# Kernel tuning notes

Measured on AMD Instinct MI355X. Metric: run time of the kernel, lower is better.

## Reference

```python
import jax, jax.numpy as jnp
import numpy as np

B = 1024          # sub (= obj) batch size
NUME = 20000      # num entities
NUMR = 8          # num relations
NET = 2 * NUMR + 1  # hetero edge types: r, -r, self
DIMT = 28         # time encoding dim
DIME = 100        # entity embedding dim
DIM = 200         # emb module output dim
H = 4             # history length
HEADS = 4         # GAT heads
OH = DIM // HEADS # GAT per-head out dim
N0 = 160000       # layer-0 src nodes
N1 = 40000        # layer-0 dst / layer-1 src nodes
R = 2 * B * H     # unique roots = layer-1 dst nodes
E0 = 60000        # edges per etype, layer 0
E1 = 16000        # edges per etype, layer 1
K = 500000        # copy mask entries
DIMR = 100        # relation embedding dim
HATT = 4          # self-attention heads
OA = DIM // HATT  # per-head q/k/v dim (Attention out_dim//h)
DIN0 = DIME + DIMT
DIN1 = DIM + DIMT


def setup_inputs() -> dict:
    key = jax.random.key(0)
    ks = jax.random.split(key, 48)
    ri = jax.random.randint
    nrm = lambda i, shp, s=0.05: jax.random.normal(ks[i], shp, jnp.float32) * s
    d = {}
    d['sub'] = ri(ks[0], (B,), 0, NUME)
    d['obj'] = ri(ks[1], (B,), 0, NUME)
    d['rel'] = ri(ks[2], (B,), 0, NUMR)
    d['ts'] = 1000
    d['nid0'] = ri(ks[3], (N0,), 0, NUME * 1000)
    d['root_idx'] = ri(ks[4], (2 * B * H,), 0, R)
    d['src0'] = ri(ks[5], (NET, E0), 0, N0)
    d['dst0'] = ri(ks[6], (NET, E0), 0, N1)
    d['src1'] = ri(ks[7], (NET, E1), 0, N1)
    d['dst1'] = ri(ks[8], (NET, E1), 0, R)
    d['copy_rows'] = ri(ks[9], (K,), 0, 2 * B)
    d['copy_cols'] = ri(ks[10], (K,), 0, NUME)
    # parameters
    d['emb_table'] = nrm(11, (NUME, DIME))
    d['time_freq'] = jnp.asarray(1.0 / 10 ** np.linspace(0, 9, DIMT), jnp.float32)
    d['time_phase'] = jnp.zeros((DIMT,), jnp.float32)
    d['Wg0'] = nrm(12, (NET, DIN0, HEADS, OH))
    d['al0'] = nrm(13, (NET, HEADS, OH))
    d['ar0'] = nrm(14, (NET, HEADS, OH))
    d['bg0'] = jnp.zeros((NET, DIM), jnp.float32)
    d['Wg1'] = nrm(15, (NET, DIN1, HEADS, OH))
    d['al1'] = nrm(16, (NET, HEADS, OH))
    d['ar1'] = nrm(17, (NET, HEADS, OH))
    d['bg1'] = jnp.zeros((NET, DIM), jnp.float32)
    d['ln0_w'] = jnp.ones((H * DIM,), jnp.float32)
    d['ln0_b'] = jnp.zeros((H * DIM,), jnp.float32)
    d['Wq'] = nrm(18, (HATT, DIM, OA))
    d['bq'] = jnp.zeros((HATT, OA), jnp.float32)
    d['Wv'] = nrm(19, (HATT, DIM, OA))
    d['bv'] = jnp.zeros((HATT, OA), jnp.float32)
    d['ln1_w'] = jnp.ones((H * DIM,), jnp.float32)
    d['ln1_b'] = jnp.zeros((H * DIM,), jnp.float32)
    d['Wd1'] = nrm(20, (H * DIM, DIM))
    d['bd1'] = jnp.zeros((DIM,), jnp.float32)
    d['srel_emb'] = nrm(21, (NUMR, DIMR))
    d['orel_emb'] = nrm(22, (NUMR, DIMR))
    d['Wsub'] = nrm(23, (DIM + DIMR, NUME))
    d['bsub'] = jnp.zeros((NUME,), jnp.float32)
    d['Wobj'] = nrm(24, (DIM + DIMR, NUME))
    d['bobj'] = jnp.zeros((NUME,), jnp.float32)
    d['csrel_emb'] = nrm(25, (NUMR, DIMR))
    d['corel_emb'] = nrm(26, (NUMR, DIMR))
    d['cWsub'] = nrm(27, (DIM + DIMR, NUME))
    d['cbsub'] = jnp.zeros((NUME,), jnp.float32)
    d['cWobj'] = nrm(28, (DIM + DIMR, NUME))
    d['cbobj'] = jnp.zeros((NUME,), jnp.float32)
    return d


def _temb(nid, ts, tf, tp):
    t = (ts - nid // NUME).astype(jnp.float32)
    return jnp.cos(t[:, None] * tf + tp)


def _gat(x, Wg, al, ar, bg, src, dst, nd):
    # heterogeneous GATConv over NET relation types, mean-aggregated (DGL HeteroGraphConv)
    msg = jnp.zeros((nd, HEADS, OH), x.dtype)
    for r in range(NET):
        s, d = src[r], dst[r]
        fs = jnp.einsum('ei,iho->eho', x[s], Wg[r])                     # [E,h,o] src feats per edge
        er_n = (jnp.einsum('ni,iho->nho', x[:nd], Wg[r]) * ar[r]).sum(-1)  # [nd,h]
        el = (fs * al[r]).sum(-1)                                       # [E,h]
        e = jax.nn.leaky_relu(el + er_n[d], 0.2)
        m = jax.ops.segment_max(e, d, num_segments=nd)
        a = jnp.exp(e - m[d])
        z = jax.ops.segment_sum(a, d, num_segments=nd)
        alpha = a / z[d]
        msg = msg + jax.ops.segment_sum(alpha[:, :, None] * fs, d, num_segments=nd)
    return jax.nn.relu((msg.reshape(nd, HEADS * OH) + bg.sum(0)) / NET)


def _ln(x, w, b):
    mu = x.mean(-1, keepdims=True)
    v = ((x - mu) ** 2).mean(-1, keepdims=True)
    return (x - mu) / jnp.sqrt(v + 1e-5) * w + b


def reference(sub, obj, rel, ts, nid0, root_idx, src0, dst0, src1, dst1, copy_rows, copy_cols, emb_table, time_freq, time_phase, Wg0, al0, ar0, bg0, Wg1, al1, ar1, bg1, ln0_w, ln0_b, Wq, bq, Wv, bv, ln1_w, ln1_b, Wd1, bd1, srel_emb, orel_emb, Wsub, bsub, Wobj, bobj, csrel_emb, corel_emb, cWsub, cbsub, cWobj, cbobj):
    # --- EmbModule: entity emb + time enc + 2-layer hetero GAT over sampled blocks ---
    h = emb_table[nid0 % NUME]                                   # [N0, DIME]
    x = jnp.concatenate([h, _temb(nid0, ts, time_freq, time_phase)], 1)
    h = _gat(x, Wg0, al0, ar0, bg0, src0, dst0, N1)              # [N1, DIM]
    x = jnp.concatenate([h, _temb(nid0[:N1], ts, time_freq, time_phase)], 1)
    h = _gat(x, Wg1, al1, ar1, bg1, src1, dst1, R)               # [R, DIM]
    hid = h[root_idx].reshape(2 * B, H * DIM)                    # [2B, H*DIM]
    # --- Copy mechanism (on detached last-history embedding) ---
    ch = jax.lax.stop_gradient(hid[:, -DIM:])
    raw_sub = jnp.concatenate([ch[B:], corel_emb[rel]], 1) @ cWsub + cbsub
    raw_obj = jnp.concatenate([ch[:B], csrel_emb[rel]], 1) @ cWobj + cbobj
    raw = jnp.concatenate([raw_sub, raw_obj], 0)                 # [2B, NUME]
    masked = jnp.full((2 * B, NUME), -100.0, raw.dtype).at[copy_rows, copy_cols].set(raw[copy_rows, copy_cols])
    csub, cobj = masked[:B], masked[B:]
    # --- Gen layers: LN -> SelfAttention -> LN -> dense ---
    x = _ln(hid, ln0_w, ln0_b)
    xs = x.reshape(2 * B, H, DIM)
    q = jnp.einsum('bse,heo->bhso', xs, Wq) + bq[:, None, :]     # k == q (w_q reused in source)
    att = jax.nn.softmax(jnp.einsum('bhso,bhto->bhst', q, q), axis=2)  # torch softmax(dim=1)
    v = jnp.einsum('bse,heo->bhso', xs, Wv) + bv[:, None, :]
    ans = jnp.einsum('bhst,bhto->bhso', att, v)                  # [2B,h,S,OA]
    x = jax.nn.relu(ans.transpose(0, 2, 1, 3).reshape(2 * B, H * DIM))
    x = _ln(x, ln1_w, ln1_b)
    x = jax.nn.relu(x @ Wd1 + bd1)                               # [2B, DIM]
    sub_emb, obj_emb = x[:B], x[B:]
    sub_pred = jnp.concatenate([obj_emb, orel_emb[rel]], 1) @ Wsub + bsub
    obj_pred = jnp.concatenate([sub_emb, srel_emb[rel]], 1) @ Wobj + bobj
    return (sub_pred, obj_pred, csub, cobj)
```

## Files before the change

kernel.cpp:

```cpp
#include <hip/hip_runtime.h>
#include <hip/hip_bf16.h>
#include <math.h>

typedef __hip_bfloat16 bf16;
typedef __attribute__((ext_vector_type(8))) short short8;
typedef __attribute__((ext_vector_type(4))) float f32x4;

#define BQ 1024
#define NUME 20000
#define NET 17
#define DIMT 28
#define DIME 100
#define DIM 200
#define HEADS 4
#define OH 50
#define N0 160000
#define N1 40000
#define RNODES 8192
#define E0 60000
#define E1 16000
#define KK 500000
#define DIMR 100
#define HATT 4
#define OA 50
// ... 54 lines not shown
  if (i >= nwords) return;
  unsigned* p = (unsigned*)((char*)outb + (size_t)2*BQ*NUME * (f32m ? 4 : 2));
  p[i] = f32m ? 0xC2C80000u : 0xC2C8C2C8u;
}

__global__ __launch_bounds__(256) void k_prep_w(const bf16* Wg, const bf16* al, const bf16* ar,
                                                float* wal, float* war, int DIN){
  int idx = blockIdx.x*256 + threadIdx.x;
  int total = NET*DIN*4;
  if (idx >= total) return;
  int h = idx & 3; int ri = idx >> 2; int i = ri % DIN; int r = ri / DIN;
  const bf16* wrow = Wg + ((size_t)(r*DIN + i))*HEADS*OH + h*OH;
  const bf16* alr = al + (size_t)(r*HEADS + h)*OH;
  const bf16* arr = ar + (size_t)(r*HEADS + h)*OH;
  float sl=0.f, sr=0.f;
  for (int o=0;o<OH;o++){ float w=b2f(wrow[o]); sl += w*b2f(alr[o]); sr += w*b2f(arr[o]); }
  wal[idx]=sl; war[idx]=sr;
}

__global__ __launch_bounds__(256) void k_pack(const bf16* Wg, bf16* wpk, int DIN, int KS){
  int idx = blockIdx.x*256 + threadIdx.x;
  int total = NET*KS*13*512;
  if (idx >= total) return;
  int j = idx & 7, lane = (idx>>3) & 63;
  int rem = idx >> 9;
  int nt = rem % 13, rks = rem / 13;
  int ks = rks % KS, r = rks / KS;
  int k = ks*32 + (lane>>4)*8 + j;
  int n = nt*16 + (lane&15);
  bf16 v = f2b(0.f);
  if (k < DIN && n < 200) v = Wg[((size_t)r*DIN + k)*200 + n];
  wpk[idx] = v;
}

__global__ __launch_bounds__(256) void k_pack_walr(const float* wal, const float* war, bf16* wpkE,
                                                   int DIN, int KS){
  int idx = blockIdx.x*256 + threadIdx.x;
  int total = KS*9*512;
  if (idx >= total) return;
  int j = idx & 7, lane = (idx>>3) & 63;
  int rem = idx >> 9;
  int nt = rem % 9, ks = rem / 9;
  int k = ks*32 + (lane>>4)*8 + j;
  int c = nt*16 + (lane&15);
  float v = 0.f;
  if (k < DIN && c < TABW){
    int r = c >> 3, q = c & 7;
    const float* wsrc = (q < 4) ? wal : war;
    v = wsrc[((size_t)r*DIN + k)*4 + (q & 3)];
  }
  wpkE[idx] = f2b(v);
}

template<int DIN, int KS>
__global__ __launch_bounds__(256) void k_elr(const bf16* __restrict__ x, const bf16* __restrict__ wpkE,
                                             float* __restrict__ tab){
  constexpr int KM = KS*32;
  constexpr int SR = KM + 8;
  __shared__ bf16 xs[64*SR];
  int rb = blockIdx.x*64;
  int t = threadIdx.x;
  constexpr int CH = KM/4;
  for (int c = t; c < 64*CH; c += 256){
    int m = c / CH, j4 = c % CH;
    uint2 v = make_uint2(0u,0u);
    if (j4*4 < DIN) v = *(const uint2*)(x + (size_t)(rb+m)*DIN + j4*4);
    *(uint2*)(xs + m*SR + j4*4) = v;
  }
  __syncthreads();
  int lane = t & 63, w = t >> 6;
  int n_idx = lane & 15, quad = lane >> 4;
  const short8* wp8 = (const short8*)wpkE;
  for (int mt=0; mt<4; mt++){
    short8 a[KS];
    const bf16* ab = xs + (size_t)(mt*16 + n_idx)*SR + quad*8;
    #pragma unroll
    for (int ks=0; ks<KS; ks++) a[ks] = *(const short8*)(ab + ks*32);
    int m = rb + mt*16 + n_idx;
    for (int nt=w; nt<9; nt+=4){
      const short8* bp = wp8 + (size_t)nt*64 + lane;
      f32x4 acc = {0.f,0.f,0.f,0.f};
      #pragma unroll
      for (int ks=0; ks<KS; ks++){
        short8 b = bp[(size_t)ks*9*64];
        acc = __builtin_amdgcn_mfma_f32_16x16x32_bf16(b, a[ks], acc, 0, 0, 0);
      }
      int nbase = nt*16 + quad*4;
      if (nbase < TABW){
        float4 o; o.x=acc[0]; o.y=acc[1]; o.z=acc[2]; o.w=acc[3];
        *(float4*)(tab + (size_t)m*TABW + nbase) = o;
      }
    }
  }
}

__global__ __launch_bounds__(256) void k_edge_lite(const float* __restrict__ tab,
                                                   const int* __restrict__ src, const int* __restrict__ dst,
                                                   bf16* abuf, float* z, int nE, int nd){
  int idx = blockIdx.x*256 + threadIdx.x;
  if (idx >= NET*nE) return;
  int r = idx / nE;
  int s = src[idx], d = dst[idx];
  float4 el = *(const float4*)(tab + (size_t)s*TABW + r*8);
  float4 er = *(const float4*)(tab + (size_t)d*TABW + r*8 + 4);
  float ev[4] = {el.x+er.x, el.y+er.y, el.z+er.z, el.w+er.w};
  float* zp = z + ((size_t)r*nd + d)*4;
// ... 64 lines not shown
    float a = expf(fminf(v, 80.f));
    ao[h] = f2b(a);
    atomicAdd(&zp[h], a);
  }
}

__global__ __launch_bounds__(256) void k_count2(const int* __restrict__ dst, int nE, int nd, unsigned* cnt){
  int i = blockIdx.x*256 + threadIdx.x;
  if (i >= NET*nE) return;
  int r = i / nE; int d = dst[i];
  atomicAdd(&cnt[(size_t)r*nd + d], 1u);
}

__global__ __launch_bounds__(256) void k_scan2(const unsigned* __restrict__ cnt, unsigned* offs, unsigned* cur,
                                               int nd, int nE, int nEpad){
  __shared__ unsigned part[256];
  int r = blockIdx.x, t = threadIdx.x;
  unsigned base = (unsigned)(r*nEpad);
  const unsigned* c = cnt + (size_t)r*nd;
  unsigned* o  = offs + (size_t)r*(nd+1);
  unsigned* cu = cur  + (size_t)r*(nd+1);
  int chunk = (nd + 255)/256;
  int lo = t*chunk, hi = lo+chunk; if (hi > nd) hi = nd; if (lo > nd) lo = nd;
  unsigned s = 0;
  for (int i=lo;i<hi;i++) s += c[i];
  part[t] = s;
  __syncthreads();
  if (t==0){ unsigned run=0; for (int i=0;i<256;i++){ unsigned v=part[i]; part[i]=run; run+=v; } }
  __syncthreads();
  unsigned run = base + part[t];
  for (int i=lo;i<hi;i++){ o[i]=run; cu[i]=run; run += c[i]; }
  if (t==0) o[nd] = base + (unsigned)nE;
}

__global__ __launch_bounds__(256) void k_fillcsr2(const int* __restrict__ dst, int nE, int nd,
                                                  unsigned* cur, int* ids){
  int i = blockIdx.x*256 + threadIdx.x;
  if (i >= NET*nE) return;
  int r = i / nE, e = i - r*nE;
  int d = dst[i];
  unsigned pos = atomicAdd(&cur[(size_t)r*(nd+1) + d], 1u);
  ids[pos] = e;
}

template<int DIN, int KS>
__global__ __launch_bounds__(256) void k_acc_mfma(const bf16* __restrict__ x, const bf16* __restrict__ wpk,
                                                  const bf16* __restrict__ abuf, const float* __restrict__ z,
                                                  const int* __restrict__ src, const int* __restrict__ dst,
                                                  const int* __restrict__ ids,
                                                  float* msg, bf16* fbuf, int nE, int nEpad, int nd, int mode){
  constexpr int KM = KS*32;
  constexpr int SR = KM + 8;
  __shared__ bf16 xs[64*SR];
  __shared__ float alpha_s[64*4];
  __shared__ int sdst[64], ssrc[64], sE[64];
  int r = blockIdx.y;
  int ls0 = blockIdx.x*64;
  int me = min(64, nE - ls0);
  int t = threadIdx.x;
  if (t < 64){
    int e = ls0 + t, vs=0, vd=0;
    if (t < me){
      if (mode == 1) e = ids[(size_t)r*nEpad + ls0 + t];
      vs = src[(size_t)r*nE + e];
      vd = dst[(size_t)r*nE + e];
    }
    sE[t]=e; ssrc[t]=vs; sdst[t]=vd;
  }
  __syncthreads();
  {
    int m = t>>2, h = t&3;
    float al = 0.f;
    if (m < me){
      float a = b2f(abuf[((size_t)r*nE + sE[m])*4 + h]);
      float zz = z[((size_t)r*nd + sdst[m])*4 + h];
      al = a / fmaxf(zz, 1e-30f);
    }
    alpha_s[m*4+h] = al;
  }
  constexpr int CH = KM/4;
  for (int c = t; c < 64*CH; c += 256){
    int m = c / CH, j4 = c % CH;
    uint2 v = make_uint2(0u,0u);
    if (m < me && j4*4 < DIN) v = *(const uint2*)(x + (size_t)ssrc[m]*DIN + j4*4);
    *(uint2*)(xs + m*SR + j4*4) = v;
  }
  __syncthreads();

  int lane = t & 63, w = t >> 6;
  int n_idx = lane & 15, quad = lane >> 4;
  const short8* wpk8 = (const short8*)wpk;
  for (int mt=0; mt<4; mt++){
    short8 a[KS];
    const bf16* abase = xs + (size_t)(mt*16 + n_idx)*SR + quad*8;
    #pragma unroll
    for (int ks=0; ks<KS; ks++) a[ks] = *(const short8*)(abase + ks*32);
    int m = mt*16 + n_idx;
    for (int nt=w; nt<13; nt+=4){
      const short8* bp = wpk8 + (((size_t)r*KS)*13 + nt)*64 + lane;
      f32x4 acc = {0.f,0.f,0.f,0.f};
      #pragma unroll
      for (int ks=0; ks<KS; ks++){
        short8 b = bp[(size_t)ks*13*64];
        acc = __builtin_amdgcn_mfma_f32_16x16x32_bf16(b, a[ks], acc, 0, 0, 0);
      }
      int nbase = nt*16 + quad*4;
      if (nbase < 200 && m < me){
        if (mode == 0){
          #pragma unroll
          for (int reg=0; reg<4; reg++){
            int n = nbase + reg;
            atomicAdd(&msg[(size_t)sdst[m]*200 + n], acc[reg] * alpha_s[m*4 + n/50]);
          }
        } else {
          ushort4 pk;
          { int n=nbase;   pk.x = f2bu(acc[0] * alpha_s[m*4 + n/50]); }
          { int n=nbase+1; pk.y = f2bu(acc[1] * alpha_s[m*4 + n/50]); }
          { int n=nbase+2; pk.z = f2bu(acc[2] * alpha_s[m*4 + n/50]); }
          { int n=nbase+3; pk.w = f2bu(acc[3] * alpha_s[m*4 + n/50]); }
          *(ushort4*)(fbuf + ((size_t)r*nEpad + ls0 + m)*200 + nbase) = pk;
        }
      }
    }
  }
}

__global__ __launch_bounds__(256) void k_gather2(const bf16* __restrict__ F, const unsigned* __restrict__ offs,
                                                 float* __restrict__ msg, int nd){
  int w = threadIdx.x >> 6, lane = threadIdx.x & 63;
  int d = blockIdx.x*4 + w;
  if (d >= nd) return;
  if (lane < 50){
    float a0=0.f, a1=0.f, a2=0.f, a3=0.f;
    for (int r=0; r<NET; r++){
      unsigned k0 = offs[(size_t)r*(nd+1) + d];
      unsigned k1 = offs[(size_t)r*(nd+1) + d + 1];
      for (unsigned k=k0; k<k1; k++){
        ushort4 v = *(const ushort4*)(F + (size_t)k*200 + lane*4);
        a0 += bs2f(v.x); a1 += bs2f(v.y); a2 += bs2f(v.z); a3 += bs2f(v.w);
      }
    }
    float4 o; o.x=a0; o.y=a1; o.z=a2; o.w=a3;
    *(float4*)(msg + (size_t)d*200 + lane*4) = o;
  }
}

__global__ __launch_bounds__(256) void k_bgs(const bf16* bg0, const bf16* bg1, float* bgs0, float* bgs1){
  int j = blockIdx.x*256 + threadIdx.x;
  if (j < DIM){ float s=0.f; for(int r=0;r<NET;r++) s += b2f(bg0[r*DIM+j]); bgs0[j]=s; }
  else if (j < 2*DIM){ int jj=j-DIM; float s=0.f; for(int r=0;r<NET;r++) s += b2f(bg1[r*DIM+jj]); bgs1[jj]=s; }
}

__global__ __launch_bounds__(256) void k_build_x0(const int* nid0, const int* ts_p, const bf16* emb,
                                                  const bf16* tf, const bf16* tp, bf16* x0){
  long idx = (long)blockIdx.x*256 + threadIdx.x;
  if (idx >= (long)N0*DIN0) return;
  int n = idx / DIN0, j = idx % DIN0;
  int nid = nid0[n];
  bf16 v;
  if (j < DIME) v = emb[(size_t)(nid % NUME)*DIME + j];
  else {
    float t = (float)(ts_p[0] - nid / NUME);
    int jj = j - DIME;
    v = f2b(cosf(t * b2f(tf[jj]) + b2f(tp[jj])));
  }
  x0[idx] = v;
}

__global__ __launch_bounds__(256) void k_build_x1(const int* nid0, const int* ts_p, const float* msg0,
                                                  const float* bgs0, const bf16* tf, const bf16* tp, bf16* x1){
  long idx = (long)blockIdx.x*256 + threadIdx.x;
  if (idx >= (long)N1*DIN1) return;
  int n = idx / DIN1, j = idx % DIN1;
  bf16 v;
  if (j < DIM){
    v = f2b(fmaxf((msg0[(size_t)n*DIM + j] + bgs0[j]) * (1.0f/NET), 0.0f));
  } else {
    int nid = nid0[n];
    float t = (float)(ts_p[0] - nid / NUME);
    int jj = j - DIM;
    v = f2b(cosf(t * b2f(tf[jj]) + b2f(tp[jj])));
  }
  x1[idx] = v;
}

__global__ __launch_bounds__(256) void k_hid(const float* msg1, const float* bgs1, const int* root_idx, float* hid){
  long idx = (long)blockIdx.x*256 + threadIdx.x;
  if (idx >= (long)NROWS*HD) return;
  int b = idx / HD, c = idx % HD;
  int s = c / DIM, j = c % DIM;
  int n = root_idx[b*4 + s];
  hid[idx] = fmaxf((msg1[(size_t)n*DIM + j] + bgs1[j]) * (1.0f/NET), 0.0f);
}

__global__ __launch_bounds__(256) void k_att_ln(const float* __restrict__ hid,
                                                const bf16* ln0w, const bf16* ln0b,
                                                const bf16* Wq, const bf16* bq,
                                                const bf16* Wv, const bf16* bv,
                                                const bf16* ln1w, const bf16* ln1b,
                                                float* __restrict__ x3){
  __shared__ float xs[HD], qs[HD], vs[HD], att_s[64], red[16];
  __shared__ float mu_s, rs_s;
  int b = blockIdx.x, t = threadIdx.x;
  int lane = t & 63, wid = t >> 6;
  const float* xr = hid + (size_t)b*HD;
  float s=0.f, s2=0.f;
  for (int j=t;j<HD;j+=256){ float v=xr[j]; s+=v; s2+=v*v; }
  for (int off=32; off; off>>=1){ s += __shfl_down(s,off); s2 += __shfl_down(s2,off); }
  if (lane==0){ red[wid]=s; red[8+wid]=s2; }
  __syncthreads();
  if (t==0){
    float S = red[0]+red[1]+red[2]+red[3];
    float S2 = red[8]+red[9]+red[10]+red[11];
    float mu = S * (1.0f/HD);
    float var = fmaxf(S2 * (1.0f/HD) - mu*mu, 0.f);
    mu_s = mu; rs_s = rsqrtf(var + 1e-5f);
  }
  __syncthreads();
  { float mu=mu_s, rs=rs_s;
    for (int j=t;j<HD;j+=256) xs[j] = (xr[j]-mu)*rs*b2f(ln0w[j]) + b2f(ln0b[j]); }
  __syncthreads();
  for (int idx=t; idx<HD; idx+=256){
    int ha = idx/200, srow=(idx%200)/50, o=idx%50;
    const float* xrow = xs + srow*200;
    const bf16* wq = Wq + (size_t)ha*DIM*OA + o;
    const bf16* wv = Wv + (size_t)ha*DIM*OA + o;
    float q=0.f, v=0.f;
    for (int e=0;e<DIM;e++){ float xv=xrow[e]; q += xv*b2f(wq[(size_t)e*OA]); v += xv*b2f(wv[(size_t)e*OA]); }
    qs[idx] = q + b2f(bq[ha*OA+o]);
    vs[idx] = v + b2f(bv[ha*OA+o]);
  }
  __syncthreads();
  if (t < 64){
    int ha=t>>4, srow=(t>>2)&3, tt=t&3;
    const float* qa = qs + ha*200 + srow*50;
    const float* qb = qs + ha*200 + tt*50;
    float sc=0.f;
    for (int o=0;o<50;o++) sc += qa[o]*qb[o];
    att_s[ha*16 + srow*4 + tt] = sc;
  }
  __syncthreads();
  if (t < 16){
    int ha=t>>2, tt=t&3;
    float m=-1e30f;
    for (int srow=0;srow<4;srow++) m = fmaxf(m, att_s[ha*16+srow*4+tt]);
    float ex[4]; float zz=0.f;
    for (int srow=0;srow<4;srow++){ ex[srow]=expf(att_s[ha*16+srow*4+tt]-m); zz+=ex[srow]; }
    for (int srow=0;srow<4;srow++) att_s[ha*16+srow*4+tt] = ex[srow]/zz;
  }
  __syncthreads();
  for (int idx=t; idx<HD; idx+=256){
    int ha = idx/200, srow=(idx%200)/50, o=idx%50;
    float a=0.f;
    for (int tt=0;tt<4;tt++) a += att_s[ha*16+srow*4+tt]*vs[ha*200+tt*50+o];
    xs[srow*200 + ha*50 + o] = fmaxf(a, 0.f);
  }
  __syncthreads();
  s=0.f; s2=0.f;
  for (int j=t;j<HD;j+=256){ float v=xs[j]; s+=v; s2+=v*v; }
  for (int off=32; off; off>>=1){ s += __shfl_down(s,off); s2 += __shfl_down(s2,off); }
  if (lane==0){ red[wid]=s; red[8+wid]=s2; }
  __syncthreads();
  if (t==0){
    float S = red[0]+red[1]+red[2]+red[3];
    float S2 = red[8]+red[9]+red[10]+red[11];
    float mu = S * (1.0f/HD);
    float var = fmaxf(S2 * (1.0f/HD) - mu*mu, 0.f);
    mu_s = mu; rs_s = rsqrtf(var + 1e-5f);
  }
  __syncthreads();
  { float mu=mu_s, rs=rs_s;
    for (int j=t;j<HD;j+=256) x3[(size_t)b*HD + j] = (xs[j]-mu)*rs*b2f(ln1w[j]) + b2f(ln1b[j]); }
}

__global__ __launch_bounds__(256) void k_d1(const float* x3, const bf16* Wd1, const bf16* bd1, float* x4){
  __shared__ float xs[8*HD];
  int rb = blockIdx.x*8, t = threadIdx.x;
  for (int idx=t; idx<8*HD; idx+=256) xs[idx] = x3[(size_t)rb*HD + idx];
  __syncthreads();
  if (t < DIM){
    float acc[8] = {0,0,0,0,0,0,0,0};
    for (int k=0;k<HD;k++){
      float w = b2f(Wd1[(size_t)k*DIM + t]);
      #pragma unroll
      for (int r=0;r<8;r++) acc[r] += xs[r*HD+k]*w;
    }
    float bb = b2f(bd1[t]);
    for (int r=0;r<8;r++) x4[(size_t)(rb+r)*DIM + t] = fmaxf(acc[r]+bb, 0.f);
  }
}

__global__ __launch_bounds__(256) void k_pack_pred(const void* Wsub, const void* Wobj, bf16* wpkP,
                                                    const unsigned* flagp){
  long idx = (long)blockIdx.x*256 + threadIdx.x;
  long total = (long)2*PKS*PNT*512;
  if (idx >= total) return;
  int j = (int)(idx & 7), lane = (int)((idx>>3) & 63);
  long rem = idx >> 9;
  int ntile = (int)(rem % PNT); rem /= PNT;
  int ks = (int)(rem % PKS); int page = (int)(rem / PKS);
  int k = ks*32 + (lane>>4)*8 + j;
  int n = ntile*16 + (lane&15);
  const void* W = page ? Wobj : Wsub;
  bool f32m = flagp[0] != 0u;
  float v = 0.f;
  if (k < 300) v = f32m ? ((const float*)W)[(size_t)k*NUME + n]
                        : b2f(((const bf16*)W)[(size_t)k*NUME + n]);
  wpkP[idx] = f2b(v);
}

__global__ __launch_bounds__(256) void k_prep_pred(const float* x4, const bf16* nSrel, const bf16* nOrel,
                                                    const int* rel, bf16* Apack){
  long idx = (long)blockIdx.x*256 + threadIdx.x;
  if (idx >= (long)2*1024*320) return;
  int j = (int)(idx % 320); long rem = idx/320;
  int row = (int)(rem % 1024); int page = (int)(rem / 1024);
  float v = 0.f;
  if (j < 200) v = x4[((size_t)(page==0 ? 1024+row : row))*DIM + j];
  else if (j < 300){
    const bf16* re = (page==0) ? nOrel : nSrel;
    v = b2f(re[(size_t)rel[row]*DIMR + (j-200)]);
  }
  Apack[idx] = f2b(v);
}

__global__ __launch_bounds__(256) void k_pred_mfma(const bf16* __restrict__ Apack, const bf16* __restrict__ wpkP,
                                                   const bf16* bsub, const bf16* bobj, void* outb,
                                                   const unsigned* flagp){
  constexpr int SR = 320 + 8;
  __shared__ bf16 As[64*SR];
  int page = blockIdx.z;
  int rb = blockIdx.y*64;
  int cb = blockIdx.x*16;
  int t = threadIdx.x;
  const bf16* Ap = Apack + (size_t)page*1024*320;
  for (int c=t; c<64*80; c+=256){
    int m=c/80, j4=c%80;
    *(uint2*)(As + m*SR + j4*4) = *(const uint2*)(Ap + (size_t)(rb+m)*320 + j4*4);
  }
  __syncthreads();
  int lane = t&63, w = t>>6;
  int n_idx = lane&15, quad = lane>>4;
  const short8* wp8 = (const short8*)(wpkP + (size_t)page*PKS*PNT*512);
  f32x4 acc[4][4];
  #pragma unroll
  for (int i=0;i<4;i++)
    #pragma unroll
    for (int mt=0;mt<4;mt++) acc[i][mt] = (f32x4){0.f,0.f,0.f,0.f};
  short8 bz = {0,0,0,0,0,0,0,0};
  for (int ks=0; ks<PKS; ks++){
    short8 bfr[4];
    #pragma unroll
    for (int i=0;i<4;i++){
      int ntile = cb + w + 4*i;
      bfr[i] = (ntile < PNT) ? wp8[((size_t)ks*PNT + ntile)*64 + lane] : bz;
    }
    short8 afr[4];
    #pragma unroll
    for (int mt=0;mt<4;mt++) afr[mt] = *(const short8*)(As + (size_t)(mt*16 + n_idx)*SR + ks*32 + quad*8);
    #pragma unroll
    for (int i=0;i<4;i++)
      #pragma unroll
      for (int mt=0;mt<4;mt++)
        acc[i][mt] = __builtin_amdgcn_mfma_f32_16x16x32_bf16(afr[mt], bfr[i], acc[i][mt], 0, 0, 0);
  }
  bool f32m = flagp[0] != 0u;
  const bf16* bias = page ? bobj : bsub;
  size_t elem_off = (size_t)page*BQ*NUME;
  for (int i=0;i<4;i++){
    int ntile = cb + w + 4*i;
    if (ntile >= PNT) continue;
    int n = ntile*16 + n_idx;
    float bb = b2f(bias[n]);
    #pragma unroll
    for (int mt=0;mt<4;mt++){
      #pragma unroll
      for (int reg=0;reg<4;reg++){
        int m = rb + mt*16 + quad*4 + reg;
        size_t oi = elem_off + (size_t)m*NUME + n;
        float val = acc[i][mt][reg] + bb;
        if (f32m) ((float*)outb)[oi] = val; else ((bf16*)outb)[oi] = f2b(val);
      }
    }
  }
}

__global__ __launch_bounds__(256) void k_pred(const float* xemb, const bf16* relemb, const int* rel,
                                              const void* W, const bf16* bias, void* outb, size_t elem_off,
                                              const unsigned* flagp){
  __shared__ float As[16*304];
  bool f32m = flagp[0] != 0u;
  int rb = blockIdx.y*16;
  int cb = blockIdx.x*512;
  int t = threadIdx.x;
  for (int idx=t; idx<16*300; idx+=256){
    int r = idx/300, i = idx%300;
    int row = rb + r;
    float v = (i < DIM) ? xemb[(size_t)row*DIM + i]
                        : b2f(relemb[(size_t)rel[row]*DIMR + (i-DIM)]);
    As[r*304+i] = v;
  }
  __syncthreads();
  int c0 = cb + t, c1 = cb + 256 + t;
  bool g0 = c0 < NUME, g1 = c1 < NUME;
  float acc0[16], acc1[16];
  #pragma unroll
  for (int r=0;r<16;r++){ acc0[r]=0.f; acc1[r]=0.f; }
  if (f32m){
    const float* W32 = (const float*)W;
    for (int k=0;k<300;k++){
      float w0 = g0 ? W32[(size_t)k*NUME + c0] : 0.f;
      float w1 = g1 ? W32[(size_t)k*NUME + c1] : 0.f;
      #pragma unroll
      for (int r=0;r<16;r++){ float a = As[r*304+k]; acc0[r] += a*w0; acc1[r] += a*w1; }
    }
  } else {
    const bf16* W16 = (const bf16*)W;
    for (int k=0;k<300;k++){
      float w0 = g0 ? b2f(W16[(size_t)k*NUME + c0]) : 0.f;
      float w1 = g1 ? b2f(W16[(size_t)k*NUME + c1]) : 0.f;
      #pragma unroll
      for (int r=0;r<16;r++){ float a = As[r*304+k]; acc0[r] += a*w0; acc1[r] += a*w1; }
    }
  }
  #pragma unroll
  for (int rr=0; rr<2; rr++){
    int c = rr ? c1 : c0;
    float* acc = rr ? acc1 : acc0;
    if (c < NUME){
      float bb = b2f(bias[c]);
      for (int r=0;r<16;r++){
        size_t oi = elem_off + (size_t)(rb+r)*NUME + c;
        float val = acc[r] + bb;
        if (f32m) ((float*)outb)[oi] = val; else ((bf16*)outb)[oi] = f2b(val);
      }
    }
  }
}

__global__ __launch_bounds__(256) void k_transpose(const void* in, bf16* out, int rows, int cols,
                                                   const unsigned* flagp){
  __shared__ bf16 tile[32][33];
  bool f32m = flagp[0] != 0u;
  int c0 = blockIdx.x*32, r0 = blockIdx.y*32;
  int tx = threadIdx.x % 32, ty = threadIdx.x / 32;
  for (int rr=ty; rr<32; rr+=8){
    int r = r0+rr, c = c0+tx;
    if (r<rows && c<cols){
      size_t i = (size_t)r*cols + c;
      tile[rr][tx] = f32m ? f2b(((const float*)in)[i]) : ((const bf16*)in)[i];
    }
// ... 32 lines not shown
  for (int i=lane; i<300; i+=64){
    float a = (i < DIM) ? chrow[i] : b2f(re[i-DIM]);
    s += a * b2f(wt[i]);
  }
  for (int off=32; off; off>>=1) s += __shfl_down(s, off);
  if (lane==0){
    size_t oi = (size_t)2*BQ*NUME + (size_t)row*NUME + col;
    float val = s + bias_v;
    if (f32m) ((float*)outb)[oi] = val; else ((bf16*)outb)[oi] = f2b(val);
  }
}

static inline dim3 GS(long n){ return dim3((unsigned)((n + 255)/256)); }

extern "C" void kernel_launch(void* const* d_in, const int* in_sizes, int n_in,
                              void* d_out, int out_size, void* d_ws, size_t ws_size,
                              hipStream_t stream){
  const int* rel       = (const int*)d_in[2];
  const int* ts_p      = (const int*)d_in[3];
  const int* nid0      = (const int*)d_in[4];
  const int* root_idx  = (const int*)d_in[5];
  const int* src0      = (const int*)d_in[6];
  const int* dst0      = (const int*)d_in[7];
  const int* src1      = (const int*)d_in[8];
  const int* dst1      = (const int*)d_in[9];
  const int* copy_rows = (const int*)d_in[10];
  const int* copy_cols = (const int*)d_in[11];
  const void* Wsub  = d_in[35];
  const void* Wobj  = d_in[37];
  const void* cWsub = d_in[41];
  const void* cWobj = d_in[43];

  char* base = (char*)d_ws;
  size_t off = 0;
  auto alloc = [&](size_t bytes)->char*{
    char* p = base + off; off = (off + bytes + 255) & ~(size_t)255; return p;
  };
  unsigned* flagp = (unsigned*)alloc(256);
  long cvt_total = 0; for (int i=0;i<CVT_NREG;i++) cvt_total += CVT_N[i];
  bf16* normb = (bf16*)alloc((size_t)cvt_total*2);
  bf16* x0    = (bf16*)alloc((size_t)N0*DIN0*2);
  bf16* x1    = (bf16*)alloc((size_t)N1*DIN1*2);
  float* msg0 = (float*)alloc((size_t)N1*DIM*4);
  float* wal0 = (float*)alloc((size_t)NET*DIN0*4*4);
  float* war0 = (float*)alloc((size_t)NET*DIN0*4*4);
  float* wal1 = (float*)alloc((size_t)NET*DIN1*4*4);
  float* war1 = (float*)alloc((size_t)NET*DIN1*4*4);
  float* bgs0 = (float*)alloc(DIM*4);
  float* bgs1 = (float*)alloc(DIM*4);
  bf16* wpk0  = (bf16*)alloc((size_t)NET*4*13*512*2);
  bf16* wpk1  = (bf16*)alloc((size_t)NET*8*13*512*2);
  bf16* wpkE0 = (bf16*)alloc((size_t)4*9*512*2);
  bf16* wpkE1 = (bf16*)alloc((size_t)8*9*512*2);
  size_t arena = off;
  char* P1 = base + arena;
  bf16*  a0b = (bf16*)P1;
  float* z0  = (float*)(P1 + (size_t)NET*E0*8);
  size_t ext1 = (size_t)NET*E0*8 + (size_t)NET*N1*16;
  char* A = base + arena;
  bf16*  a1b  = (bf16*)A;
  float* z1   = (float*)(A + (size_t)NET*E1*8);
  size_t msg1_off = (size_t)NET*E1*8 + (size_t)NET*RNODES*16;
  float* msg1 = (float*)(A + msg1_off);
  size_t hid_off = msg1_off + (size_t)RNODES*DIM*4;
  float* hid  = (float*)(A + hid_off);
  size_t x3_off = hid_off + (size_t)NROWS*HD*4;
  float* x3   = (float*)(A + x3_off);
  float* x4   = (float*)(A + x3_off + (size_t)NROWS*HD*4);
  size_t ext2 = x3_off + (size_t)NROWS*HD*4 + (size_t)NROWS*DIM*4;
  bf16* cWsubT = (bf16*)x0;
  bf16* cWobjT = (bf16*)((char*)x0 + (size_t)NUME*300*2);

  size_t extmax = ext1 > ext2 ? ext1 : ext2;
  size_t tail = (arena + extmax + 255) & ~(size_t)255;
  size_t cnt_sz  = (((size_t)NET*N1*4) + 255) & ~(size_t)255;
  size_t offs_sz = (((size_t)NET*(N1+1)*4) + 255) & ~(size_t)255;
  size_t ids_sz  = (((size_t)NET*E0PAD*4) + 255) & ~(size_t)255;
  unsigned* cnt  = (unsigned*)(base + tail);
  unsigned* offs = (unsigned*)(base + tail + cnt_sz);
  unsigned* cur  = (unsigned*)(base + tail + cnt_sz + offs_sz);
  int* ids = (int*)(base + tail + cnt_sz + 2*offs_sz);
  size_t F_off = tail + cnt_sz + 2*offs_sz + ids_sz;
  bf16* fbuf = (bf16*)(base + F_off);
  size_t fcap = (ws_size > F_off) ? (ws_size - F_off) : 0;
  bool sortok0 = fcap >= (size_t)NET*E0PAD*400;
  bool sortok1 = fcap >= (size_t)NET*E1PAD*400;
  float* tab0 = (float*)fbuf;
  float* tab1 = (float*)fbuf;
  bool elrok0 = fcap >= (size_t)N0*TABW*4;
  bool elrok1 = fcap >= (size_t)N1*TABW*4;
  bf16* er0f = (bf16*)x1;
  bf16* er1f = (bf16*)x0;
  size_t wpkP_sz = (size_t)2*PKS*PNT*512*2;
  size_t Apack_sz = (size_t)2*1024*320*2;
  bf16* wpkP  = (bf16*)(base + F_off);
  bf16* Apack = (bf16*)(base + F_off + wpkP_sz);
  bool predok = fcap >= (wpkP_sz + Apack_sz);

  long cum[CVT_NREG+1]; cum[0]=0;
  for (int i=0;i<CVT_NREG;i++) cum[i+1] = cum[i] + CVT_N[i];
  auto NP = [&](int i)->const bf16*{ return normb + cum[i]; };
  const bf16 *nEmb=NP(0), *nTf=NP(1), *nTp=NP(2), *nWg0=NP(3), *nAl0=NP(4), *nAr0=NP(5), *nBg0=NP(6),
             *nWg1=NP(7), *nAl1=NP(8), *nAr1=NP(9), *nBg1=NP(10), *nLn0w=NP(11), *nLn0b=NP(12),
             *nWq=NP(13), *nBq=NP(14), *nWv=NP(15), *nBv=NP(16), *nLn1w=NP(17), *nLn1b=NP(18),
             *nWd1=NP(19), *nBd1=NP(20), *nSrel=NP(21), *nOrel=NP(22), *nBsub=NP(23), *nBobj=NP(24),
             *nCsrel=NP(25), *nCorel=NP(26), *nCbsub=NP(27), *nCbobj=NP(28);

  k_detect<<<dim3(1),64,0,stream>>>((const unsigned*)d_in[13], flagp);
  CvtSrcs srcs;
  for (int i=0;i<CVT_NREG;i++) srcs.p[i] = d_in[CVT_DIN[i]];
  CvtMeta meta;
  { int c=0, bc=0;
    for (int i=0;i<CVT_NREG;i++){ meta.cum[i]=c; meta.bcum[i]=bc; c+=CVT_N[i]; bc += (CVT_N[i]+255)/256; }
    meta.cum[CVT_NREG]=c; meta.bcum[CVT_NREG]=bc;
    k_cvt<<<dim3((unsigned)bc),256,0,stream>>>(srcs, meta, normb, flagp);
  }
  k_fill_u32<<<GS((long)NET*N1*4),256,0,stream>>>((unsigned*)z0, 0u, (long)NET*N1*4);
  k_fill_out<<<GS((long)2*BQ*NUME),256,0,stream>>>(d_out, flagp);
  k_prep_w<<<GS(NET*DIN0*4),256,0,stream>>>(nWg0, nAl0, nAr0, wal0, war0, DIN0);
  k_prep_w<<<GS(NET*DIN1*4),256,0,stream>>>(nWg1, nAl1, nAr1, wal1, war1, DIN1);
  k_pack<<<GS((long)NET*4*13*512),256,0,stream>>>(nWg0, wpk0, DIN0, 4);
  k_pack<<<GS((long)NET*8*13*512),256,0,stream>>>(nWg1, wpk1, DIN1, 8);
  k_pack_walr<<<GS((long)4*9*512),256,0,stream>>>(wal0, war0, wpkE0, DIN0, 4);
  k_pack_walr<<<GS((long)8*9*512),256,0,stream>>>(wal1, war1, wpkE1, DIN1, 8);
  k_bgs<<<GS(2*DIM),256,0,stream>>>(nBg0, nBg1, bgs0, bgs1);
  k_build_x0<<<GS((long)N0*DIN0),256,0,stream>>>(nid0, ts_p, nEmb, nTf, nTp, x0);

  if (elrok0){
    k_elr<DIN0,4><<<dim3(N0/64),256,0,stream>>>(x0, wpkE0, tab0);
    k_edge_lite<<<GS((long)NET*E0),256,0,stream>>>(tab0, src0, dst0, a0b, z0, E0, N1);
  } else {
    k_er<DIN0><<<GS((long)NET*N1),256,0,stream>>>(x0, war0, er0f, N1);
    k_edge<DIN0><<<GS((long)NET*E0),256,0,stream>>>(x0, wal0, er0f, src0, dst0, a0b, z0, E0, N1);
  }
  if (sortok0){
    k_fill_u32<<<GS((long)NET*N1),256,0,stream>>>(cnt, 0u, (long)NET*N1);
    k_count2<<<GS((long)NET*E0),256,0,stream>>>(dst0, E0, N1, cnt);
    k_scan2<<<dim3(NET),256,0,stream>>>(cnt, offs, cur, N1, E0, E0PAD);
    k_fillcsr2<<<GS((long)NET*E0),256,0,stream>>>(dst0, E0, N1, cur, ids);
    k_acc_mfma<DIN0,4><<<dim3((E0+63)/64, NET),256,0,stream>>>(x0, wpk0, a0b, z0, src0, dst0, ids,
                                                                msg0, fbuf, E0, E0PAD, N1, 1);
    k_gather2<<<dim3((N1+3)/4),256,0,stream>>>(fbuf, offs, msg0, N1);
  } else {
    k_fill_u32<<<GS((long)N1*DIM),256,0,stream>>>((unsigned*)msg0, 0u, (long)N1*DIM);
    k_acc_mfma<DIN0,4><<<dim3((E0+63)/64, NET),256,0,stream>>>(x0, wpk0, a0b, z0, src0, dst0, (int*)nullptr,
                                                                msg0, (bf16*)nullptr, E0, E0, N1, 0);
  }

  k_build_x1<<<GS((long)N1*DIN1),256,0,stream>>>(nid0, ts_p, msg0, bgs0, nTf, nTp, x1);
  k_fill_u32<<<GS((long)NET*RNODES*4),256,0,stream>>>((unsigned*)z1, 0u, (long)NET*RNODES*4);
  if (elrok1){
    k_elr<DIN1,8><<<dim3(N1/64),256,0,stream>>>(x1, wpkE1, tab1);
    k_edge_lite<<<GS((long)NET*E1),256,0,stream>>>(tab1, src1, dst1, a1b, z1, E1, RNODES);
  } else {
    k_er<DIN1><<<GS((long)NET*RNODES),256,0,stream>>>(x1, war1, er1f, RNODES);
    k_edge<DIN1><<<GS((long)NET*E1),256,0,stream>>>(x1, wal1, er1f, src1, dst1, a1b, z1, E1, RNODES);
  }
  if (sortok1){
    k_fill_u32<<<GS((long)NET*RNODES),256,0,stream>>>(cnt, 0u, (long)NET*RNODES);
    k_count2<<<GS((long)NET*E1),256,0,stream>>>(dst1, E1, RNODES, cnt);
    k_scan2<<<dim3(NET),256,0,stream>>>(cnt, offs, cur, RNODES, E1, E1PAD);
    k_fillcsr2<<<GS((long)NET*E1),256,0,stream>>>(dst1, E1, RNODES, cur, ids);
    k_acc_mfma<DIN1,8><<<dim3((E1+63)/64, NET),256,0,stream>>>(x1, wpk1, a1b, z1, src1, dst1, ids,
                                                                msg1, fbuf, E1, E1PAD, RNODES, 1);
    k_gather2<<<dim3((RNODES+3)/4),256,0,stream>>>(fbuf, offs, msg1, RNODES);
  } else {
    k_fill_u32<<<GS((long)RNODES*DIM),256,0,stream>>>((unsigned*)msg1, 0u, (long)RNODES*DIM);
    k_acc_mfma<DIN1,8><<<dim3((E1+63)/64, NET),256,0,stream>>>(x1, wpk1, a1b, z1, src1, dst1, (int*)nullptr,
                                                                msg1, (bf16*)nullptr, E1, E1, RNODES, 0);
  }

  if (predok)
    k_pack_pred<<<GS((long)2*PKS*PNT*512),256,0,stream>>>(Wsub, Wobj, wpkP, flagp);

  k_hid<<<GS((long)NROWS*HD),256,0,stream>>>(msg1, bgs1, root_idx, hid);
  k_transpose<<<dim3(625,10),256,0,stream>>>(cWsub, cWsubT, 300, NUME, flagp);
  k_transpose<<<dim3(625,10),256,0,stream>>>(cWobj, cWobjT, 300, NUME, flagp);
  k_scatter<<<dim3((KK+3)/4),256,0,stream>>>(copy_rows, copy_cols, rel, hid, nCsrel, nCorel,
                                             cWsubT, cWobjT, nCbsub, nCbobj, d_out, flagp);

  k_att_ln<<<dim3(NROWS),256,0,stream>>>(hid, nLn0w, nLn0b, nWq, nBq, nWv, nBv, nLn1w, nLn1b, x3);
  k_d1<<<dim3(NROWS/8),256,0,stream>>>(x3, nWd1, nBd1, x4);

  if (predok){
    k_prep_pred<<<GS((long)2*1024*320),256,0,stream>>>(x4, nSrel, nOrel, rel, Apack);
    k_pred_mfma<<<dim3(79,16,2),256,0,stream>>>(Apack, wpkP, nBsub, nBobj, d_out, flagp);
  } else {
    k_pred<<<dim3(40,64),256,0,stream>>>(x4 + (size_t)BQ*DIM, nOrel, rel, Wsub, nBsub, d_out, 0, flagp);
    k_pred<<<dim3(40,64),256,0,stream>>>(x4,                  nSrel, rel, Wobj, nBobj, d_out, (size_t)BQ*NUME, flagp);
  }
  (void)in_sizes; (void)n_in; (void)out_size; (void)ws_size;
}
```

Before: 2.279 ms.

## Move attention Q/V and dense projection to MFMA GEMMs; stage edge features via LDS

Splits the fused per-row attention kernel into a LayerNorm-to-bf16 pass, an MFMA GEMM for the Q and V projections, a small attention kernel, and an MFMA GEMM for the dense layer, with weights prepacked into MFMA fragment layout. This replaces scalar per-row dot products that reread the weights for every row. Edge-feature writes in the CSR accumulate kernel are staged through shared memory so global stores are coalesced 16-byte rows. Intermediates now pass through bf16 buffers, which lowers precision, and the extra kernel launches and memory round trips add overhead.

```diff
diff --git a/kernel.cpp b/kernel.cpp
--- a/kernel.cpp
+++ b/kernel.cpp
@@ -130,6 +130,38 @@
   wpkE[idx] = f2b(v);
 }
 
+__global__ __launch_bounds__(256) void k_pack_qv(const bf16* Wq, const bf16* Wv, bf16* wpkQV){
+  int idx = blockIdx.x*256 + threadIdx.x;
+  int total = 2*8*13*512;
+  if (idx >= total) return;
+  int j = idx & 7, lane = (idx>>3) & 63;
+  int rem = idx >> 9;
+  int nt = rem % 13; rem /= 13;
+  int ks = rem % 8; int gy = rem / 8;
+  int k = ks*32 + (lane>>4)*8 + j;
+  int n = nt*16 + (lane&15);
+  bf16 v = f2b(0.f);
+  if (k < 200 && n < 200){
+    const bf16* W = gy ? Wv : Wq;
+    v = W[(size_t)(n/50)*10000 + (size_t)k*50 + (n%50)];
+  }
+  wpkQV[idx] = v;
+}
+
+__global__ __launch_bounds__(256) void k_pack_d1(const bf16* Wd1, bf16* wpkD1){
+  int idx = blockIdx.x*256 + threadIdx.x;
+  int total = 28*13*512;
+  if (idx >= total) return;
+  int j = idx & 7, lane = (idx>>3) & 63;
+  int rem = idx >> 9;
+  int nt = rem % 13; int ks = rem / 13;
+  int k = ks*32 + (lane>>4)*8 + j;
+  int n = nt*16 + (lane&15);
+  bf16 v = f2b(0.f);
+  if (k < 800 && n < 200) v = Wd1[(size_t)k*200 + n];
+  wpkD1[idx] = v;
+}
+
 template<int DIN, int KS>
 __global__ __launch_bounds__(256) void k_elr(const bf16* __restrict__ x, const bf16* __restrict__ wpkE,
                                              float* __restrict__ tab){
@@ -300,6 +332,7 @@
   constexpr int KM = KS*32;
   constexpr int SR = KM + 8;
   __shared__ bf16 xs[64*SR];
+  __shared__ bf16 fs[16*208];
   __shared__ float alpha_s[64*4];
   __shared__ int sdst[64], ssrc[64], sE[64];
   int r = blockIdx.y;
@@ -366,9 +399,18 @@
           { int n=nbase+1; pk.y = f2bu(acc[1] * alpha_s[m*4 + n/50]); }
           { int n=nbase+2; pk.z = f2bu(acc[2] * alpha_s[m*4 + n/50]); }
           { int n=nbase+3; pk.w = f2bu(acc[3] * alpha_s[m*4 + n/50]); }
-          *(ushort4*)(fbuf + ((size_t)r*nEpad + ls0 + m)*200 + nbase) = pk;
+          *(ushort4*)(fs + (size_t)n_idx*208 + nbase) = pk;
         }
       }
+    }
+    if (mode == 1){
+      __syncthreads();
+      for (int ii=t; ii<400; ii+=256){
+        int rw = ii/25, cc = ii%25;
+        *(uint4*)(fbuf + ((size_t)r*nEpad + ls0 + mt*16 + rw)*200 + cc*8) =
+            *(const uint4*)(fs + (size_t)rw*208 + cc*8);
+      }
+      __syncthreads();
     }
   }
 }
@@ -441,23 +483,18 @@
   hid[idx] = fmaxf((msg1[(size_t)n*DIM + j] + bgs1[j]) * (1.0f/NET), 0.0f);
 }
 
-__global__ __launch_bounds__(256) void k_att_ln(const float* __restrict__ hid,
-                                                const bf16* ln0w, const bf16* ln0b,
-                                                const bf16* Wq, const bf16* bq,
-                                                const bf16* Wv, const bf16* bv,
-                                                const bf16* ln1w, const bf16* ln1b,
-                                                float* __restrict__ x3){
-  __shared__ float xs[HD], qs[HD], vs[HD], att_s[64], red[16];
+__global__ __launch_bounds__(256) void k_ln_bf16(const float* xin, const bf16* w, const bf16* b, bf16* xout){
+  int row = blockIdx.x;
+  const float* xr = xin + (size_t)row*HD;
+  __shared__ float red[16];
   __shared__ float mu_s, rs_s;
-  int b = blockIdx.x, t = threadIdx.x;
-  int lane = t & 63, wid = t >> 6;
-  const float* xr = hid + (size_t)b*HD;
   float s=0.f, s2=0.f;
-  for (int j=t;j<HD;j+=256){ float v=xr[j]; s+=v; s2+=v*v; }
+  for (int j=threadIdx.x;j<HD;j+=256){ float v=xr[j]; s+=v; s2+=v*v; }
   for (int off=32; off; off>>=1){ s += __shfl_down(s,off); s2 += __shfl_down(s2,off); }
+  int lane = threadIdx.x & 63, wid = threadIdx.x >> 6;
   if (lane==0){ red[wid]=s; red[8+wid]=s2; }
   __syncthreads();
-  if (t==0){
+  if (threadIdx.x==0){
     float S = red[0]+red[1]+red[2]+red[3];
     float S2 = red[8]+red[9]+red[10]+red[11];
     float mu = S * (1.0f/HD);
@@ -465,24 +502,91 @@
     mu_s = mu; rs_s = rsqrtf(var + 1e-5f);
   }
   __syncthreads();
-  { float mu=mu_s, rs=rs_s;
-    for (int j=t;j<HD;j+=256) xs[j] = (xr[j]-mu)*rs*b2f(ln0w[j]) + b2f(ln0b[j]); }
-  __syncthreads();
-  for (int idx=t; idx<HD; idx+=256){
-    int ha = idx/200, srow=(idx%200)/50, o=idx%50;
-    const float* xrow = xs + srow*200;
-    const bf16* wq = Wq + (size_t)ha*DIM*OA + o;
-    const bf16* wv = Wv + (size_t)ha*DIM*OA + o;
-    float q=0.f, v=0.f;
-    for (int e=0;e<DIM;e++){ float xv=xrow[e]; q += xv*b2f(wq[(size_t)e*OA]); v += xv*b2f(wv[(size_t)e*OA]); }
-    qs[idx] = q + b2f(bq[ha*OA+o]);
-    vs[idx] = v + b2f(bv[ha*OA+o]);
+  float mu = mu_s, rs = rs_s;
+  for (int j=threadIdx.x;j<HD;j+=256){
+    float v = (xr[j]-mu)*rs;
+    xout[(size_t)row*HD + j] = f2b(v*b2f(w[j]) + b2f(b[j]));
+  }
+}
+
+__global__ __launch_bounds__(256) void k_qv_mfma(const bf16* __restrict__ xlnb, const bf16* __restrict__ wpkQV,
+                                                 const bf16* bq, const bf16* bv, float* __restrict__ qv){
+  constexpr int SR = 136;
+  __shared__ bf16 xs[64*SR];
+  int rb = blockIdx.x*64;
+  int gy = blockIdx.y;
+  int t = threadIdx.x;
+  int lane = t&63, w = t>>6;
+  int n_idx = lane&15, quad = lane>>4;
+  f32x4 acc[4][4];
+  #pragma unroll
+  for (int i=0;i<4;i++)
+    #pragma unroll
+    for (int mt=0;mt<4;mt++) acc[i][mt] = (f32x4){0.f,0.f,0.f,0.f};
+  const short8* wp8 = (const short8*)(wpkQV + (size_t)gy*8*13*512);
+  short8 bz = {0,0,0,0,0,0,0,0};
+  for (int c=0;c<2;c++){
+    for (int ci=t; ci<64*32; ci+=256){
+      int m = ci>>5, j4 = ci&31;
+      int gcol = c*128 + j4*4;
+      uint2 v = make_uint2(0u,0u);
+      if (gcol < 200) v = *(const uint2*)(xlnb + (size_t)(rb+m)*200 + gcol);
+      *(uint2*)(xs + m*SR + j4*4) = v;
+    }
+    __syncthreads();
+    for (int ks=0; ks<4; ks++){
+      short8 bfr[4];
+      #pragma unroll
+      for (int i=0;i<4;i++){
+        int nt = w + 4*i;
+        bfr[i] = (nt < 13) ? wp8[(((size_t)(c*4+ks))*13 + nt)*64 + lane] : bz;
+      }
+      short8 afr[4];
+      #pragma unroll
+      for (int mt=0;mt<4;mt++) afr[mt] = *(const short8*)(xs + (size_t)(mt*16+n_idx)*SR + ks*32 + quad*8);
+      #pragma unroll
+      for (int i=0;i<4;i++)
+        #pragma unroll
+        for (int mt=0;mt<4;mt++)
+          acc[i][mt] = __builtin_amdgcn_mfma_f32_16x16x32_bf16(afr[mt], bfr[i], acc[i][mt], 0, 0, 0);
+    }
+    __syncthreads();
+  }
+  const bf16* bias = gy ? bv : bq;
+  for (int i=0;i<4;i++){
+    int nt = w + 4*i;
+    if (nt >= 13) continue;
+    int n = nt*16 + n_idx;
+    if (n >= 200) continue;
+    float bb = b2f(bias[n]);
+    #pragma unroll
+    for (int mt=0;mt<4;mt++){
+      #pragma unroll
+      for (int reg=0;reg<4;reg++){
+        int m = rb + mt*16 + quad*4 + reg;
+        qv[(size_t)m*400 + gy*200 + n] = acc[i][mt][reg] + bb;
+      }
+    }
+  }
+}
+
+__global__ __launch_bounds__(256) void k_att2(const float* __restrict__ qv,
+                                              const bf16* ln1w, const bf16* ln1b,
+                                              bf16* __restrict__ x3b){
+  __shared__ float qs[HD], vs[HD], xs2[HD], att_s[64], red[16];
+  __shared__ float mu_s, rs_s;
+  int b = blockIdx.x, t = threadIdx.x;
+  int lane = t & 63, wid = t >> 6;
+  for (int idx=t; idx<1600; idx+=256){
+    int s = idx/400, c = idx%400;
+    float v = qv[((size_t)(b*4+s))*400 + c];
+    if (c < 200) qs[s*200+c] = v; else vs[s*200 + c-200] = v;
   }
   __syncthreads();
   if (t < 64){
     int ha=t>>4, srow=(t>>2)&3, tt=t&3;
-    const float* qa = qs + ha*200 + srow*50;
-    const float* qb = qs + ha*200 + tt*50;
+    const float* qa = qs + srow*200 + ha*50;
+    const float* qb = qs + tt*200 + ha*50;
     float sc=0.f;
     for (int o=0;o<50;o++) sc += qa[o]*qb[o];
     att_s[ha*16 + srow*4 + tt] = sc;
@@ -498,14 +602,14 @@
   }
   __syncthreads();
   for (int idx=t; idx<HD; idx+=256){
-    int ha = idx/200, srow=(idx%200)/50, o=idx%50;
+    int srow = idx/200, ha = (idx%200)/50, o = idx%50;
     float a=0.f;
-    for (int tt=0;tt<4;tt++) a += att_s[ha*16+srow*4+tt]*vs[ha*200+tt*50+o];
-    xs[srow*200 + ha*50 + o] = fmaxf(a, 0.f);
-  }
-  __syncthreads();
-  s=0.f; s2=0.f;
-  for (int j=t;j<HD;j+=256){ float v=xs[j]; s+=v; s2+=v*v; }
+    for (int tt=0;tt<4;tt++) a += att_s[ha*16+srow*4+tt]*vs[tt*200+ha*50+o];
+    xs2[idx] = fmaxf(a, 0.f);
+  }
+  __syncthreads();
+  float s=0.f, s2=0.f;
+  for (int j=t;j<HD;j+=256){ float v=xs2[j]; s+=v; s2+=v*v; }
   for (int off=32; off; off>>=1){ s += __shfl_down(s,off); s2 += __shfl_down(s2,off); }
   if (lane==0){ red[wid]=s; red[8+wid]=s2; }
   __syncthreads();
@@ -518,23 +622,65 @@
   }
   __syncthreads();
   { float mu=mu_s, rs=rs_s;
-    for (int j=t;j<HD;j+=256) x3[(size_t)b*HD + j] = (xs[j]-mu)*rs*b2f(ln1w[j]) + b2f(ln1b[j]); }
-}
-
-__global__ __launch_bounds__(256) void k_d1(const float* x3, const bf16* Wd1, const bf16* bd1, float* x4){
-  __shared__ float xs[8*HD];
-  int rb = blockIdx.x*8, t = threadIdx.x;
-  for (int idx=t; idx<8*HD; idx+=256) xs[idx] = x3[(size_t)rb*HD + idx];
-  __syncthreads();
-  if (t < DIM){
-    float acc[8] = {0,0,0,0,0,0,0,0};
-    for (int k=0;k<HD;k++){
-      float w = b2f(Wd1[(size_t)k*DIM + t]);
-      #pragma unroll
-      for (int r=0;r<8;r++) acc[r] += xs[r*HD+k]*w;
-    }
-    float bb = b2f(bd1[t]);
-    for (int r=0;r<8;r++) x4[(size_t)(rb+r)*DIM + t] = fmaxf(acc[r]+bb, 0.f);
+    for (int j=t;j<HD;j+=256) x3b[(size_t)b*HD + j] = f2b((xs2[j]-mu)*rs*b2f(ln1w[j]) + b2f(ln1b[j])); }
+}
+
+__global__ __launch_bounds__(256) void k_d1_mfma(const bf16* __restrict__ x3b, const bf16* __restrict__ wpkD1,
+                                                 const bf16* bd1, bf16* __restrict__ x4b){
+  constexpr int SR = 136;
+  __shared__ bf16 xs[64*SR];
+  int rb = blockIdx.x*64;
+  int t = threadIdx.x;
+  int lane = t&63, w = t>>6;
+  int n_idx = lane&15, quad = lane>>4;
+  f32x4 acc[4][4];
+  #pragma unroll
+  for (int i=0;i<4;i++)
+    #pragma unroll
+    for (int mt=0;mt<4;mt++) acc[i][mt] = (f32x4){0.f,0.f,0.f,0.f};
+  const short8* wp8 = (const short8*)wpkD1;
+  short8 bz = {0,0,0,0,0,0,0,0};
+  for (int c=0;c<7;c++){
+    for (int ci=t; ci<64*32; ci+=256){
+      int m = ci>>5, j4 = ci&31;
+      int gcol = c*128 + j4*4;
+      uint2 v = make_uint2(0u,0u);
+      if (gcol < 800) v = *(const uint2*)(x3b + (size_t)(rb+m)*800 + gcol);
+      *(uint2*)(xs + m*SR + j4*4) = v;
+    }
+    __syncthreads();
+    for (int ks=0; ks<4; ks++){
+      short8 bfr[4];
+      #pragma unroll
+      for (int i=0;i<4;i++){
+        int nt = w + 4*i;
+        bfr[i] = (nt < 13) ? wp8[(((size_t)(c*4+ks))*13 + nt)*64 + lane] : bz;
+      }
+      short8 afr[4];
+      #pragma unroll
+      for (int mt=0;mt<4;mt++) afr[mt] = *(const short8*)(xs + (size_t)(mt*16+n_idx)*SR + ks*32 + quad*8);
+      #pragma unroll
+      for (int i=0;i<4;i++)
+        #pragma unroll
+        for (int mt=0;mt<4;mt++)
+          acc[i][mt] = __builtin_amdgcn_mfma_f32_16x16x32_bf16(afr[mt], bfr[i], acc[i][mt], 0, 0, 0);
+    }
+    __syncthreads();
+  }
+  for (int i=0;i<4;i++){
+    int nt = w + 4*i;
+    if (nt >= 13) continue;
+    int n = nt*16 + n_idx;
+    if (n >= 200) continue;
+    float bb = b2f(bd1[n]);
+    #pragma unroll
+    for (int mt=0;mt<4;mt++){
+      #pragma unroll
+      for (int reg=0;reg<4;reg++){
+        int m = rb + mt*16 + quad*4 + reg;
+        x4b[(size_t)m*200 + n] = f2b(fmaxf(acc[i][mt][reg] + bb, 0.f));
+      }
+    }
   }
 }
 
@@ -557,19 +703,19 @@
   wpkP[idx] = f2b(v);
 }
 
-__global__ __launch_bounds__(256) void k_prep_pred(const float* x4, const bf16* nSrel, const bf16* nOrel,
+__global__ __launch_bounds__(256) void k_prep_pred(const bf16* x4b, const bf16* nSrel, const bf16* nOrel,
                                                     const int* rel, bf16* Apack){
   long idx = (long)blockIdx.x*256 + threadIdx.x;
   if (idx >= (long)2*1024*320) return;
   int j = (int)(idx % 320); long rem = idx/320;
   int row = (int)(rem % 1024); int page = (int)(rem / 1024);
-  float v = 0.f;
-  if (j < 200) v = x4[((size_t)(page==0 ? 1024+row : row))*DIM + j];
+  bf16 v = f2b(0.f);
+  if (j < 200) v = x4b[((size_t)(page==0 ? 1024+row : row))*DIM + j];
   else if (j < 300){
     const bf16* re = (page==0) ? nOrel : nSrel;
-    v = b2f(re[(size_t)rel[row]*DIMR + (j-200)]);
-  }
-  Apack[idx] = f2b(v);
+    v = re[(size_t)rel[row]*DIMR + (j-200)];
+  }
+  Apack[idx] = v;
 }
 
 __global__ __launch_bounds__(256) void k_pred_mfma(const bf16* __restrict__ Apack, const bf16* __restrict__ wpkP,
@@ -633,7 +779,7 @@
   }
 }
 
-__global__ __launch_bounds__(256) void k_pred(const float* xemb, const bf16* relemb, const int* rel,
+__global__ __launch_bounds__(256) void k_pred(const bf16* xemb, const bf16* relemb, const int* rel,
                                               const void* W, const bf16* bias, void* outb, size_t elem_off,
                                               const unsigned* flagp){
   __shared__ float As[16*304];
@@ -644,7 +790,7 @@
   for (int idx=t; idx<16*300; idx+=256){
     int r = idx/300, i = idx%300;
     int row = rb + r;
-    float v = (i < DIM) ? xemb[(size_t)row*DIM + i]
+    float v = (i < DIM) ? b2f(xemb[(size_t)row*DIM + i])
                         : b2f(relemb[(size_t)rel[row]*DIMR + (i-DIM)]);
     As[r*304+i] = v;
   }
@@ -783,6 +929,8 @@
   bf16* wpk1  = (bf16*)alloc((size_t)NET*8*13*512*2);
   bf16* wpkE0 = (bf16*)alloc((size_t)4*9*512*2);
   bf16* wpkE1 = (bf16*)alloc((size_t)8*9*512*2);
+  bf16* wpkQV = (bf16*)alloc((size_t)2*8*13*512*2);
+  bf16* wpkD1 = (bf16*)alloc((size_t)28*13*512*2);
   size_t arena = off;
   char* P1 = base + arena;
   bf16*  a0b = (bf16*)P1;
@@ -795,10 +943,15 @@
   float* msg1 = (float*)(A + msg1_off);
   size_t hid_off = msg1_off + (size_t)RNODES*DIM*4;
   float* hid  = (float*)(A + hid_off);
-  size_t x3_off = hid_off + (size_t)NROWS*HD*4;
-  float* x3   = (float*)(A + x3_off);
-  float* x4   = (float*)(A + x3_off + (size_t)NROWS*HD*4);
-  size_t ext2 = x3_off + (size_t)NROWS*HD*4 + (size_t)NROWS*DIM*4;
+  size_t xlnb_off = hid_off + (size_t)NROWS*HD*4;
+  bf16* xlnb = (bf16*)(A + xlnb_off);
+  size_t qv_off = xlnb_off + (size_t)NROWS*HD*2;
+  float* qvb = (float*)(A + qv_off);
+  size_t x3b_off = qv_off + (size_t)NROWS*4*400*4;
+  bf16* x3b = (bf16*)(A + x3b_off);
+  size_t x4b_off = x3b_off + (size_t)NROWS*HD*2;
+  bf16* x4b = (bf16*)(A + x4b_off);
+  size_t ext2 = x4b_off + (size_t)NROWS*DIM*2;
   bf16* cWsubT = (bf16*)x0;
   bf16* cWobjT = (bf16*)((char*)x0 + (size_t)NUME*300*2);
 
@@ -854,6 +1007,8 @@
   k_pack<<<GS((long)NET*8*13*512),256,0,stream>>>(nWg1, wpk1, DIN1, 8);
   k_pack_walr<<<GS((long)4*9*512),256,0,stream>>>(wal0, war0, wpkE0, DIN0, 4);
   k_pack_walr<<<GS((long)8*9*512),256,0,stream>>>(wal1, war1, wpkE1, DIN1, 8);
+  k_pack_qv<<<GS((long)2*8*13*512),256,0,stream>>>(nWq, nWv, wpkQV);
+  k_pack_d1<<<GS((long)28*13*512),256,0,stream>>>(nWd1, wpkD1);
   k_bgs<<<GS(2*DIM),256,0,stream>>>(nBg0, nBg1, bgs0, bgs1);
   k_build_x0<<<GS((long)N0*DIN0),256,0,stream>>>(nid0, ts_p, nEmb, nTf, nTp, x0);
 
@@ -910,15 +1065,17 @@
   k_scatter<<<dim3((KK+3)/4),256,0,stream>>>(copy_rows, copy_cols, rel, hid, nCsrel, nCorel,
                                              cWsubT, cWobjT, nCbsub, nCbobj, d_out, flagp);
 
-  k_att_ln<<<dim3(NROWS),256,0,stream>>>(hid, nLn0w, nLn0b, nWq, nBq, nWv, nBv, nLn1w, nLn1b, x3);
-  k_d1<<<dim3(NROWS/8),256,0,stream>>>(x3, nWd1, nBd1, x4);
+  k_ln_bf16<<<dim3(NROWS),256,0,stream>>>(hid, nLn0w, nLn0b, xlnb);
+  k_qv_mfma<<<dim3(NROWS*4/64, 2),256,0,stream>>>(xlnb, wpkQV, nBq, nBv, qvb);
+  k_att2<<<dim3(NROWS),256,0,stream>>>(qvb, nLn1w, nLn1b, x3b);
+  k_d1_mfma<<<dim3(NROWS/64),256,0,stream>>>(x3b, wpkD1, nBd1, x4b);
 
   if (predok){
-    k_prep_pred<<<GS((long)2*1024*320),256,0,stream>>>(x4, nSrel, nOrel, rel, Apack);
+    k_prep_pred<<<GS((long)2*1024*320),256,0,stream>>>(x4b, nSrel, nOrel, rel, Apack);
     k_pred_mfma<<<dim3(79,16,2),256,0,stream>>>(Apack, wpkP, nBsub, nBobj, d_out, flagp);
   } else {
-    k_pred<<<dim3(40,64),256,0,stream>>>(x4 + (size_t)BQ*DIM, nOrel, rel, Wsub, nBsub, d_out, 0, flagp);
-    k_pred<<<dim3(40,64),256,0,stream>>>(x4,                  nSrel, rel, Wobj, nBobj, d_out, (size_t)BQ*NUME, flagp);
+    k_pred<<<dim3(40,64),256,0,stream>>>(x4b + (size_t)BQ*DIM, nOrel, rel, Wsub, nBsub, d_out, 0, flagp);
+    k_pred<<<dim3(40,64),256,0,stream>>>(x4b,                  nSrel, rel, Wobj, nBobj, d_out, (size_t)BQ*NUME, flagp);
   }
   (void)in_sizes; (void)n_in; (void)out_size; (void)ws_size;
 }
```

Measured after the change: 2.144 ms. 5.9% less time.
